# Optimization experiments

Hardware: AMD Instinct MI355X
Metric: run time of the kernel (lower is better)

The kernel has to match this reference:

```python
import jax, jax.numpy as jnp
import numpy as np

N_NODES = 100000
N_EDGES = 1600000
D_IN = 128
D_OUT = 128


def setup_inputs() -> dict:
    key = jax.random.key(0)
    k_x, k_w, k_r, k_c, k_v = jax.random.split(key, 5)
    x = jax.random.normal(k_x, (N_NODES, D_IN), dtype=jnp.float32)
    # xavier_uniform: U(-a, a), a = sqrt(6/(fan_in+fan_out))
    a = float(np.sqrt(6.0 / (D_IN + D_OUT)))
    W = jax.random.uniform(k_w, (D_IN, D_OUT), dtype=jnp.float32, minval=-a, maxval=a)
    edge_row = jax.random.randint(k_r, (N_EDGES,), 0, N_NODES, dtype=jnp.int32)
    edge_col = jax.random.randint(k_c, (N_EDGES,), 0, N_NODES, dtype=jnp.int32)
    edge_val = jax.random.uniform(k_v, (N_EDGES,), dtype=jnp.float32)
    return {"x": x, "W": W, "edge_row": edge_row, "edge_col": edge_col, "edge_val": edge_val}


def reference(x, W, edge_row, edge_col, edge_val):
    # dropout with p=0.0 is the identity (module default), so omitted.
    support = x @ W                                  # [N, D_OUT] dense GEMM
    # sparse adj @ support in COO form: out[r] += v * support[c]
    msgs = support[edge_col] * edge_val[:, None]      # [E, D_OUT] irregular gather
    out = jax.ops.segment_sum(msgs, edge_row, num_segments=x.shape[0])
    return jnp.tanh(out)
```

## Files before the change

kernel.cpp:

```cpp
#include <hip/hip_runtime.h>
#include <hip/hip_bf16.h>
#include <hip/hip_fp16.h>
#include <math.h>

#define D 128
#define BIN_SHIFT 8
#define BIN_ROWS 256
#define NB_MAX 512
#define CPAD 16
#define AW 4096

typedef _Float16 half8 __attribute__((ext_vector_type(8)));
typedef float floatx4 __attribute__((ext_vector_type(4)));
typedef float floatx2 __attribute__((ext_vector_type(2)));

__global__ void gcn_wt_kernel(const float* __restrict__ W,
                              unsigned short* __restrict__ wt,
                              int* __restrict__ cbin) {
    const int i = blockIdx.x * 256 + threadIdx.x;
    const int n = i >> 7, k = i & 127;
    wt[i] = __half_as_ushort(__float2half_rn(W[k * D + n]));
    if (blockIdx.x < 2) cbin[blockIdx.x * 256 + threadIdx.x] = 0;
}

__global__ __launch_bounds__(256) void gcn_gemm_kernel(
        const float* __restrict__ x, const unsigned short* __restrict__ wt,
        unsigned short* __restrict__ support2, int n_nodes) {
    const int wave = threadIdx.x >> 6;
    const int lane = threadIdx.x & 63;
    const int q = lane >> 4;
    const int n16 = lane & 15;
    const int row_base = blockIdx.x * 128 + wave * 32;
    if (row_base >= n_nodes) return;

    const half8* wt8 = (const half8*)wt;

    floatx4 acc[2][8];
#pragma unroll
    for (int mt = 0; mt < 2; ++mt)
#pragma unroll
        for (int nt = 0; nt < 8; ++nt) acc[mt][nt] = (floatx4){0.f, 0.f, 0.f, 0.f};

#pragma unroll
    for (int kc = 0; kc < 4; ++kc) {
        half8 b[8];
#pragma unroll
        for (int nt = 0; nt < 8; ++nt)
            b[nt] = wt8[(nt * 16 + n16) * 16 + kc * 4 + q];
#pragma unroll
        for (int mt = 0; mt < 2; ++mt) {
            const float* xp = x + (size_t)(row_base + mt * 16 + n16) * D
                                + kc * 32 + q * 8;
            const float4 f0 = *(const float4*)xp;
            const float4 f1 = *(const float4*)(xp + 4);
            half8 a;
            a[0] = (_Float16)f0.x; a[1] = (_Float16)f0.y;
            a[2] = (_Float16)f0.z; a[3] = (_Float16)f0.w;
            a[4] = (_Float16)f1.x; a[5] = (_Float16)f1.y;
            a[6] = (_Float16)f1.z; a[7] = (_Float16)f1.w;
#pragma unroll
            for (int nt = 0; nt < 8; ++nt)
                acc[mt][nt] = __builtin_amdgcn_mfma_f32_16x16x32_f16(
                    a, b[nt], acc[mt][nt], 0, 0, 0);
        }
    }

#pragma unroll
    for (int mt = 0; mt < 2; ++mt) {
        const int r0 = row_base + mt * 16 + q * 4;
#pragma unroll
        for (int nt = 0; nt < 8; ++nt) {
            const int col = nt * 16 + n16;
#pragma unroll
            for (int i = 0; i < 4; ++i)
                support2[(size_t)(r0 + i) * D + col] =
                    __half_as_ushort(__float2half_rn(acc[mt][nt][i]));
        }
    }
}

__global__ __launch_bounds__(256) void gcn_chist_kernel(
        const int* __restrict__ erow, int* __restrict__ cbin, int n_edges) {
    __shared__ int h[NB_MAX];
    const int t = threadIdx.x;
    h[t] = 0;
    h[t + 256] = 0;
    __syncthreads();
    const int stride = gridDim.x * 256 * 4;
    const int nv = n_edges & ~3;
    for (int i = (blockIdx.x * 256 + t) * 4; i + 3 < n_edges; i += stride) {
        const int4 r = *(const int4*)(erow + i);
        atomicAdd(&h[r.x >> BIN_SHIFT], 1);
        atomicAdd(&h[r.y >> BIN_SHIFT], 1);
        atomicAdd(&h[r.z >> BIN_SHIFT], 1);
        atomicAdd(&h[r.w >> BIN_SHIFT], 1);
    }
    if (blockIdx.x == 0) {
        for (int i = nv + t; i < n_edges; i += 256)
            atomicAdd(&h[erow[i] >> BIN_SHIFT], 1);
    }
    __syncthreads();
    if (h[t] > 0) atomicAdd(&cbin[t], h[t]);
    if (h[t + 256] > 0) atomicAdd(&cbin[t + 256], h[t + 256]);
}

__global__ __launch_bounds__(512) void gcn_cscan_kernel(
        const int* __restrict__ cbin, int* __restrict__ cbase,
        int* __restrict__ ccur, int* __restrict__ offsets,
        int nbins, int n_nodes, int n_edges) {
    __shared__ int sm[512];
    const int t = threadIdx.x;
    const int v = (t < nbins) ? cbin[t] : 0;
    sm[t] = v;
    __syncthreads();
    for (int off = 1; off < 512; off <<= 1) {
        int tv = (t >= off) ? sm[t - off] : 0;
        __syncthreads();
        sm[t] += tv;
        __syncthreads();
    }
    const int ex = sm[t] - v;
    if (t < nbins) { cbase[t] = ex; ccur[t * CPAD] = ex; }
    if (t == 0) { cbase[nbins] = n_edges; offsets[n_nodes] = n_edges; }
}

__global__ __launch_bounds__(512) void gcn_binA_kernel(
        const int* __restrict__ erow, const int* __restrict__ ecol,
        const float* __restrict__ eval, int* __restrict__ ccur,
        uint2* __restrict__ tmp8, int n_edges, int nbins) {
    __shared__ uint2 recs[AW];
    __shared__ int hist[NB_MAX];
    __shared__ int lstart[NB_MAX];
    __shared__ int gbase[NB_MAX];
    const int t = threadIdx.x;
    const int w0 = blockIdx.x * AW;
    const int wend = min(w0 + AW, n_edges);
    const int cnt = wend - w0;

    hist[t] = 0;
    __syncthreads();

    for (int i = w0 + t; i < wend; i += 512)
        atomicAdd(&hist[erow[i] >> BIN_SHIFT], 1);
    __syncthreads();

    {
        const int v = hist[t];
        gbase[t] = v;
        __syncthreads();
        for (int off = 1; off < 512; off <<= 1) {
            int tv = (t >= off) ? gbase[t - off] : 0;
            __syncthreads();
            gbase[t] += tv;
            __syncthreads();
        }
        lstart[t] = gbase[t] - v;
        __syncthreads();
    }

    {
        const int c = hist[t];
        int gb = 0;
        if (t < nbins && c > 0) gb = atomicAdd(&ccur[t * CPAD], c);
        __syncthreads();
        gbase[t] = gb;
        hist[t] = lstart[t];
    }
    __syncthreads();

    for (int i = w0 + t; i < wend; i += 512) {
        const int r = erow[i];
        const int c = ecol[i];
        const unsigned short vh = __half_as_ushort(__float2half_rn(eval[i]));
        const int b = r >> BIN_SHIFT;
        const int p = atomicAdd(&hist[b], 1);
        recs[p] = make_uint2(((unsigned)r << 15) | vh, (unsigned)c);
    }
    __syncthreads();

    for (int s = t; s < cnt; s += 512) {
        const uint2 rec = recs[s];
        const int b = (int)(rec.x >> 15) >> BIN_SHIFT;
        tmp8[gbase[b] + (s - lstart[b])] = rec;
    }
}

__global__ __launch_bounds__(256) void gcn_binB_kernel(
        const uint2* __restrict__ tmp8, const int* __restrict__ cbase,
        int* __restrict__ offsets,
        unsigned int* __restrict__ rec4, int n_nodes) {
    __shared__ int cnt[BIN_ROWS];
    __shared__ int sm[BIN_ROWS];
    const int bin = blockIdx.x;
    const int r0 = bin << BIN_SHIFT;
    const int t = threadIdx.x;
    cnt[t] = 0;
    __syncthreads();

    const int beg = cbase[bin];
    const int end = cbase[bin + 1];

    for (int i = beg + t; i < end; i += 256)
        atomicAdd(&cnt[(int)(tmp8[i].x >> 15) - r0], 1);
    __syncthreads();

    const int v = cnt[t];
    sm[t] = v;
    __syncthreads();
    for (int off = 1; off < 256; off <<= 1) {
        int tv = (t >= off) ? sm[t - off] : 0;
        __syncthreads();
        sm[t] += tv;
        __syncthreads();
    }
    const int mypos = beg + sm[t] - v;

    const int row = r0 + t;
    if (row < n_nodes) offsets[row] = mypos;
    __syncthreads();
    cnt[t] = mypos;
    __syncthreads();

    for (int i = beg + t; i < end; i += 256) {
        const uint2 p = tmp8[i];
        const int pos = atomicAdd(&cnt[(int)(p.x >> 15) - r0], 1);
        rec4[pos] = (p.y << 15) | (p.x & 0x7FFFu);
    }
}

__global__ __launch_bounds__(256) void gcn_gather_kernel(
        const unsigned int* __restrict__ support_u,
        const unsigned int* __restrict__ rec4,
        const int* __restrict__ offsets,
        float* __restrict__ out, int n_nodes) {
    const int node = __builtin_amdgcn_readfirstlane(
        blockIdx.x * 4 + (threadIdx.x >> 6));
    const int lane = threadIdx.x & 63;
    if (node >= n_nodes) return;

    const int beg = offsets[node];
    const int end = offsets[node + 1];

    float ax = 0.f, ay = 0.f, bx = 0.f, by = 0.f;
    int e = beg;
    for (; e + 7 < end; e += 8) {
        unsigned r[8], s[8];
#pragma unroll
        for (int j = 0; j < 8; ++j) r[j] = rec4[e + j];
#pragma unroll
        for (int j = 0; j < 8; ++j)
            s[j] = support_u[(size_t)(r[j] >> 15) * 64 + lane];
#pragma unroll
        for (int j = 0; j < 8; ++j) {
            const float v = __half2float(__ushort_as_half((unsigned short)(r[j] & 0x7FFFu)));
            const float slo = __half2float(__ushort_as_half((unsigned short)(s[j] & 0xFFFFu)));
            const float shi = __half2float(__ushort_as_half((unsigned short)(s[j] >> 16)));
            if (j & 1) { bx += v * slo; by += v * shi; }
            else       { ax += v * slo; ay += v * shi; }
        }
    }
    for (; e + 3 < end; e += 4) {
        unsigned r[4], s[4];
#pragma unroll
        for (int j = 0; j < 4; ++j) r[j] = rec4[e + j];
#pragma unroll
        for (int j = 0; j < 4; ++j)
            s[j] = support_u[(size_t)(r[j] >> 15) * 64 + lane];
#pragma unroll
        for (int j = 0; j < 4; ++j) {
            const float v = __half2float(__ushort_as_half((unsigned short)(r[j] & 0x7FFFu)));
            const float slo = __half2float(__ushort_as_half((unsigned short)(s[j] & 0xFFFFu)));
            const float shi = __half2float(__ushort_as_half((unsigned short)(s[j] >> 16)));
            if (j & 1) { bx += v * slo; by += v * shi; }
            else       { ax += v * slo; ay += v * shi; }
        }
    }
    for (; e < end; ++e) {
        const unsigned r = rec4[e];
        const unsigned s = support_u[(size_t)(r >> 15) * 64 + lane];
        const float v = __half2float(__ushort_as_half((unsigned short)(r & 0x7FFFu)));
        ax += v * __half2float(__ushort_as_half((unsigned short)(s & 0xFFFFu)));
        ay += v * __half2float(__ushort_as_half((unsigned short)(s >> 16)));
    }

    floatx2 res;
    res.x = tanhf(ax + bx);
    res.y = tanhf(ay + by);
    floatx2* out2 = (floatx2*)out;
    __builtin_nontemporal_store(res, &out2[(size_t)node * 64 + lane]);
}

extern "C" void kernel_launch(void* const* d_in, const int* in_sizes, int n_in,
                              void* d_out, int out_size, void* d_ws, size_t ws_size,
                              hipStream_t stream) {
    const float* x    = (const float*)d_in[0];
    const float* W    = (const float*)d_in[1];
    const int*   erow = (const int*)d_in[2];
    const int*   ecol = (const int*)d_in[3];
    const float* eval = (const float*)d_in[4];
    float* out = (float*)d_out;

    const int n_nodes = in_sizes[0] / D;
    const int n_edges = in_sizes[2];
    const int nbins = (n_nodes + BIN_ROWS - 1) >> BIN_SHIFT;

    unsigned short* support2 = (unsigned short*)d_ws;
    unsigned short* wt = support2 + (size_t)n_nodes * D;
    uint2* tmp8   = (uint2*)(wt + D * D);
    unsigned int* rec4 = (unsigned int*)(tmp8 + n_edges);
    int*  offsets = (int*)(rec4 + n_edges);
    int*  cbin    = offsets + n_nodes + 1;
    int*  cbase   = cbin + NB_MAX;
    int*  ccur    = cbase + NB_MAX + 1;

    gcn_wt_kernel<<<(D * D) / 256, 256, 0, stream>>>(W, wt, cbin);
    gcn_gemm_kernel<<<(n_nodes + 127) / 128, 256, 0, stream>>>(
        x, wt, support2, n_nodes);

    gcn_chist_kernel<<<320, 256, 0, stream>>>(erow, cbin, n_edges);
    gcn_cscan_kernel<<<1, 512, 0, stream>>>(cbin, cbase, ccur, offsets,
                                            nbins, n_nodes, n_edges);

    gcn_binA_kernel<<<(n_edges + AW - 1) / AW, 512, 0, stream>>>(
        erow, ecol, eval, ccur, tmp8, n_edges, nbins);
    gcn_binB_kernel<<<nbins, 256, 0, stream>>>(tmp8, cbase, offsets, rec4, n_nodes);

    gcn_gather_kernel<<<(n_nodes + 3) / 4, 256, 0, stream>>>(
        (const unsigned int*)support2, rec4, offsets, out, n_nodes);
}
```

Before: 241.3 us.

## Scatter binA records directly and gather support rows as 8-byte loads per half-wave

The binning kernel drops its shared-memory staging buffer and prefix scan. Each edge record is now written straight to its global bin slot through a shared atomic cursor, using 256 threads per block. The gather kernel splits each wave into two halves that take alternate edges, and each lane loads 8 bytes (four fp16 values) instead of 4. The two halves' partial sums are combined with a cross-half shuffle before the tanh and a 16-byte store. This aims to cut the edge-loop iterations per wave in half and to shrink binA's shared-memory footprint. The cost is less coalesced scattered global writes in binA, plus an extra shuffle and idle lanes at the store in the gather.

```diff
diff --git a/kernel.cpp b/kernel.cpp
--- a/kernel.cpp
+++ b/kernel.cpp
@@ -124,64 +124,41 @@
     if (t == 0) { cbase[nbins] = n_edges; offsets[n_nodes] = n_edges; }
 }
 
-__global__ __launch_bounds__(512) void gcn_binA_kernel(
+__global__ __launch_bounds__(256) void gcn_binA_kernel(
         const int* __restrict__ erow, const int* __restrict__ ecol,
         const float* __restrict__ eval, int* __restrict__ ccur,
         uint2* __restrict__ tmp8, int n_edges, int nbins) {
-    __shared__ uint2 recs[AW];
     __shared__ int hist[NB_MAX];
-    __shared__ int lstart[NB_MAX];
-    __shared__ int gbase[NB_MAX];
+    __shared__ int base[NB_MAX];
     const int t = threadIdx.x;
     const int w0 = blockIdx.x * AW;
     const int wend = min(w0 + AW, n_edges);
-    const int cnt = wend - w0;
 
     hist[t] = 0;
-    __syncthreads();
-
-    for (int i = w0 + t; i < wend; i += 512)
+    hist[t + 256] = 0;
+    __syncthreads();
+
+    for (int i = w0 + t; i < wend; i += 256)
         atomicAdd(&hist[erow[i] >> BIN_SHIFT], 1);
     __syncthreads();
 
-    {
-        const int v = hist[t];
-        gbase[t] = v;
-        __syncthreads();
-        for (int off = 1; off < 512; off <<= 1) {
-            int tv = (t >= off) ? gbase[t - off] : 0;
-            __syncthreads();
-            gbase[t] += tv;
-            __syncthreads();
-        }
-        lstart[t] = gbase[t] - v;
-        __syncthreads();
-    }
-
-    {
-        const int c = hist[t];
-        int gb = 0;
-        if (t < nbins && c > 0) gb = atomicAdd(&ccur[t * CPAD], c);
-        __syncthreads();
-        gbase[t] = gb;
-        hist[t] = lstart[t];
-    }
-    __syncthreads();
-
-    for (int i = w0 + t; i < wend; i += 512) {
+#pragma unroll
+    for (int s = 0; s < 2; ++s) {
+        const int b = t + s * 256;
+        const int c = hist[b];
+        base[b] = (b < nbins && c > 0) ? atomicAdd(&ccur[b * CPAD], c) : 0;
+    }
+    __syncthreads();
+    hist[t] = base[t];
+    hist[t + 256] = base[t + 256];
+    __syncthreads();
+
+    for (int i = w0 + t; i < wend; i += 256) {
         const int r = erow[i];
         const int c = ecol[i];
         const unsigned short vh = __half_as_ushort(__float2half_rn(eval[i]));
-        const int b = r >> BIN_SHIFT;
-        const int p = atomicAdd(&hist[b], 1);
-        recs[p] = make_uint2(((unsigned)r << 15) | vh, (unsigned)c);
-    }
-    __syncthreads();
-
-    for (int s = t; s < cnt; s += 512) {
-        const uint2 rec = recs[s];
-        const int b = (int)(rec.x >> 15) >> BIN_SHIFT;
-        tmp8[gbase[b] + (s - lstart[b])] = rec;
+        const int pos = atomicAdd(&hist[r >> BIN_SHIFT], 1);
+        tmp8[pos] = make_uint2(((unsigned)r << 15) | vh, (unsigned)c);
     }
 }
 
@@ -236,58 +213,70 @@
     const int node = __builtin_amdgcn_readfirstlane(
         blockIdx.x * 4 + (threadIdx.x >> 6));
     const int lane = threadIdx.x & 63;
+    const int half = lane >> 5;
+    const int l32 = lane & 31;
     if (node >= n_nodes) return;
+
+    const uint2* support8 = (const uint2*)support_u;
 
     const int beg = offsets[node];
     const int end = offsets[node + 1];
 
-    float ax = 0.f, ay = 0.f, bx = 0.f, by = 0.f;
+    float a0 = 0.f, a1 = 0.f, a2 = 0.f, a3 = 0.f;
+    float b0 = 0.f, b1 = 0.f, b2 = 0.f, b3 = 0.f;
     int e = beg;
     for (; e + 7 < end; e += 8) {
-        unsigned r[8], s[8];
-#pragma unroll
-        for (int j = 0; j < 8; ++j) r[j] = rec4[e + j];
-#pragma unroll
-        for (int j = 0; j < 8; ++j)
-            s[j] = support_u[(size_t)(r[j] >> 15) * 64 + lane];
-#pragma unroll
-        for (int j = 0; j < 8; ++j) {
-            const float v = __half2float(__ushort_as_half((unsigned short)(r[j] & 0x7FFFu)));
-            const float slo = __half2float(__ushort_as_half((unsigned short)(s[j] & 0xFFFFu)));
-            const float shi = __half2float(__ushort_as_half((unsigned short)(s[j] >> 16)));
-            if (j & 1) { bx += v * slo; by += v * shi; }
-            else       { ax += v * slo; ay += v * shi; }
-        }
-    }
-    for (; e + 3 < end; e += 4) {
-        unsigned r[4], s[4];
-#pragma unroll
-        for (int j = 0; j < 4; ++j) r[j] = rec4[e + j];
+        unsigned r[4];
+        uint2 s[4];
+#pragma unroll
+        for (int j = 0; j < 4; ++j) r[j] = rec4[e + 2 * j + half];
 #pragma unroll
         for (int j = 0; j < 4; ++j)
-            s[j] = support_u[(size_t)(r[j] >> 15) * 64 + lane];
+            s[j] = support8[(size_t)(r[j] >> 15) * 32 + l32];
 #pragma unroll
         for (int j = 0; j < 4; ++j) {
             const float v = __half2float(__ushort_as_half((unsigned short)(r[j] & 0x7FFFu)));
-            const float slo = __half2float(__ushort_as_half((unsigned short)(s[j] & 0xFFFFu)));
-            const float shi = __half2float(__ushort_as_half((unsigned short)(s[j] >> 16)));
-            if (j & 1) { bx += v * slo; by += v * shi; }
-            else       { ax += v * slo; ay += v * shi; }
+            const float c0 = __half2float(__ushort_as_half((unsigned short)(s[j].x & 0xFFFFu)));
+            const float c1 = __half2float(__ushort_as_half((unsigned short)(s[j].x >> 16)));
+            const float c2 = __half2float(__ushort_as_half((unsigned short)(s[j].y & 0xFFFFu)));
+            const float c3 = __half2float(__ushort_as_half((unsigned short)(s[j].y >> 16)));
+            if (j & 1) { b0 += v * c0; b1 += v * c1; b2 += v * c2; b3 += v * c3; }
+            else       { a0 += v * c0; a1 += v * c1; a2 += v * c2; a3 += v * c3; }
         }
     }
-    for (; e < end; ++e) {
+    for (; e + 1 < end; e += 2) {
+        const unsigned r = rec4[e + half];
+        const uint2 s = support8[(size_t)(r >> 15) * 32 + l32];
+        const float v = __half2float(__ushort_as_half((unsigned short)(r & 0x7FFFu)));
+        a0 += v * __half2float(__ushort_as_half((unsigned short)(s.x & 0xFFFFu)));
+        a1 += v * __half2float(__ushort_as_half((unsigned short)(s.x >> 16)));
+        a2 += v * __half2float(__ushort_as_half((unsigned short)(s.y & 0xFFFFu)));
+        a3 += v * __half2float(__ushort_as_half((unsigned short)(s.y >> 16)));
+    }
+    if (e < end) {
         const unsigned r = rec4[e];
-        const unsigned s = support_u[(size_t)(r >> 15) * 64 + lane];
-        const float v = __half2float(__ushort_as_half((unsigned short)(r & 0x7FFFu)));
-        ax += v * __half2float(__ushort_as_half((unsigned short)(s & 0xFFFFu)));
-        ay += v * __half2float(__ushort_as_half((unsigned short)(s >> 16)));
-    }
-
-    floatx2 res;
-    res.x = tanhf(ax + bx);
-    res.y = tanhf(ay + by);
-    floatx2* out2 = (floatx2*)out;
-    __builtin_nontemporal_store(res, &out2[(size_t)node * 64 + lane]);
+        const uint2 s = support8[(size_t)(r >> 15) * 32 + l32];
+        const float v = half ? 0.f
+            : __half2float(__ushort_as_half((unsigned short)(r & 0x7FFFu)));
+        a0 += v * __half2float(__ushort_as_half((unsigned short)(s.x & 0xFFFFu)));
+        a1 += v * __half2float(__ushort_as_half((unsigned short)(s.x >> 16)));
+        a2 += v * __half2float(__ushort_as_half((unsigned short)(s.y & 0xFFFFu)));
+        a3 += v * __half2float(__ushort_as_half((unsigned short)(s.y >> 16)));
+    }
+
+    a0 += b0; a1 += b1; a2 += b2; a3 += b3;
+    a0 += __shfl_xor(a0, 32);
+    a1 += __shfl_xor(a1, 32);
+    a2 += __shfl_xor(a2, 32);
+    a3 += __shfl_xor(a3, 32);
+
+    if (half == 0) {
+        floatx4 res;
+        res.x = tanhf(a0); res.y = tanhf(a1);
+        res.z = tanhf(a2); res.w = tanhf(a3);
+        floatx4* out4 = (floatx4*)out;
+        __builtin_nontemporal_store(res, &out4[(size_t)node * 32 + l32]);
+    }
 }
 
 extern "C" void kernel_launch(void* const* d_in, const int* in_sizes, int n_in,
@@ -321,7 +310,7 @@
     gcn_cscan_kernel<<<1, 512, 0, stream>>>(cbin, cbase, ccur, offsets,
                                             nbins, n_nodes, n_edges);
 
-    gcn_binA_kernel<<<(n_edges + AW - 1) / AW, 512, 0, stream>>>(
+    gcn_binA_kernel<<<(n_edges + AW - 1) / AW, 256, 0, stream>>>(
         erow, ecol, eval, ccur, tmp8, n_edges, nbins);
     gcn_binB_kernel<<<nbins, 256, 0, stream>>>(tmp8, cbase, offsets, rec4, n_nodes);
 
```

New measurement: 265.6 us. 1.1x slower.

## Fuse per-row sort with gather into one bin kernel using LDS records

Applied to the files above, without the earlier changes.

Halves the bin size to 128 rows (782 bins) and merges the second binning pass with the gather/tanh kernel. Each block counts and scans the rows in its bin, scatters the packed edge records into shared memory (falling back to global memory when the bin exceeds LCAP), then eight waves loop over the bin's rows doing the gather. This removes the offsets array, one kernel launch, and the global write and re-read of rec4. The cost is only 782 blocks of 512 threads for the gather phase, which may limit occupancy and latency hiding compared with the earlier one-wave-per-node launch.

```diff
diff --git a/kernel.cpp b/kernel.cpp
--- a/kernel.cpp
+++ b/kernel.cpp
@@ -4,11 +4,12 @@
 #include <math.h>
 
 #define D 128
-#define BIN_SHIFT 8
-#define BIN_ROWS 256
-#define NB_MAX 512
+#define BIN_SHIFT 7
+#define BIN_ROWS 128
+#define NB_MAX 1024
 #define CPAD 16
 #define AW 4096
+#define LCAP 2560
 
 typedef _Float16 half8 __attribute__((ext_vector_type(8)));
 typedef float floatx4 __attribute__((ext_vector_type(4)));
@@ -20,7 +21,7 @@
     const int i = blockIdx.x * 256 + threadIdx.x;
     const int n = i >> 7, k = i & 127;
     wt[i] = __half_as_ushort(__float2half_rn(W[k * D + n]));
-    if (blockIdx.x < 2) cbin[blockIdx.x * 256 + threadIdx.x] = 0;
+    if (blockIdx.x < 4) cbin[blockIdx.x * 256 + threadIdx.x] = 0;
 }
 
 __global__ __launch_bounds__(256) void gcn_gemm_kernel(
@@ -83,8 +84,8 @@
         const int* __restrict__ erow, int* __restrict__ cbin, int n_edges) {
     __shared__ int h[NB_MAX];
     const int t = threadIdx.x;
-    h[t] = 0;
-    h[t + 256] = 0;
+#pragma unroll
+    for (int s = 0; s < 4; ++s) h[t + s * 256] = 0;
     __syncthreads();
     const int stride = gridDim.x * 256 * 4;
     const int nv = n_edges & ~3;
@@ -100,20 +101,22 @@
             atomicAdd(&h[erow[i] >> BIN_SHIFT], 1);
     }
     __syncthreads();
-    if (h[t] > 0) atomicAdd(&cbin[t], h[t]);
-    if (h[t + 256] > 0) atomicAdd(&cbin[t + 256], h[t + 256]);
-}
-
-__global__ __launch_bounds__(512) void gcn_cscan_kernel(
+#pragma unroll
+    for (int s = 0; s < 4; ++s) {
+        const int b = t + s * 256;
+        if (h[b] > 0) atomicAdd(&cbin[b], h[b]);
+    }
+}
+
+__global__ __launch_bounds__(1024) void gcn_cscan_kernel(
         const int* __restrict__ cbin, int* __restrict__ cbase,
-        int* __restrict__ ccur, int* __restrict__ offsets,
-        int nbins, int n_nodes, int n_edges) {
-    __shared__ int sm[512];
+        int* __restrict__ ccur, int nbins, int n_edges) {
+    __shared__ int sm[1024];
     const int t = threadIdx.x;
     const int v = (t < nbins) ? cbin[t] : 0;
     sm[t] = v;
     __syncthreads();
-    for (int off = 1; off < 512; off <<= 1) {
+    for (int off = 1; off < 1024; off <<= 1) {
         int tv = (t >= off) ? sm[t - off] : 0;
         __syncthreads();
         sm[t] += tv;
@@ -121,7 +124,7 @@
     }
     const int ex = sm[t] - v;
     if (t < nbins) { cbase[t] = ex; ccur[t * CPAD] = ex; }
-    if (t == 0) { cbase[nbins] = n_edges; offsets[n_nodes] = n_edges; }
+    if (t == 0) cbase[nbins] = n_edges;
 }
 
 __global__ __launch_bounds__(512) void gcn_binA_kernel(
@@ -132,40 +135,46 @@
     __shared__ int hist[NB_MAX];
     __shared__ int lstart[NB_MAX];
     __shared__ int gbase[NB_MAX];
+    __shared__ int sm[512];
     const int t = threadIdx.x;
     const int w0 = blockIdx.x * AW;
     const int wend = min(w0 + AW, n_edges);
     const int cnt = wend - w0;
 
     hist[t] = 0;
+    hist[t + 512] = 0;
     __syncthreads();
 
     for (int i = w0 + t; i < wend; i += 512)
         atomicAdd(&hist[erow[i] >> BIN_SHIFT], 1);
     __syncthreads();
 
-    {
-        const int v = hist[t];
-        gbase[t] = v;
-        __syncthreads();
-        for (int off = 1; off < 512; off <<= 1) {
-            int tv = (t >= off) ? gbase[t - off] : 0;
-            __syncthreads();
-            gbase[t] += tv;
-            __syncthreads();
-        }
-        lstart[t] = gbase[t] - v;
-        __syncthreads();
-    }
-
-    {
-        const int c = hist[t];
+    const int c0 = hist[2 * t], c1 = hist[2 * t + 1];
+    const int s2 = c0 + c1;
+    sm[t] = s2;
+    __syncthreads();
+    for (int off = 1; off < 512; off <<= 1) {
+        int tv = (t >= off) ? sm[t - off] : 0;
+        __syncthreads();
+        sm[t] += tv;
+        __syncthreads();
+    }
+    const int ex = sm[t] - s2;
+    lstart[2 * t] = ex;
+    lstart[2 * t + 1] = ex + c0;
+    __syncthreads();
+
+#pragma unroll
+    for (int s = 0; s < 2; ++s) {
+        const int b = 2 * t + s;
+        const int c = hist[b];
         int gb = 0;
-        if (t < nbins && c > 0) gb = atomicAdd(&ccur[t * CPAD], c);
-        __syncthreads();
-        gbase[t] = gb;
-        hist[t] = lstart[t];
-    }
+        if (b < nbins && c > 0) gb = atomicAdd(&ccur[b * CPAD], c);
+        gbase[b] = gb;
+    }
+    __syncthreads();
+    hist[2 * t] = lstart[2 * t];
+    hist[2 * t + 1] = lstart[2 * t + 1];
     __syncthreads();
 
     for (int i = w0 + t; i < wend; i += 512) {
@@ -185,109 +194,102 @@
     }
 }
 
-__global__ __launch_bounds__(256) void gcn_binB_kernel(
+__global__ __launch_bounds__(512) void gcn_gatherB_kernel(
         const uint2* __restrict__ tmp8, const int* __restrict__ cbase,
-        int* __restrict__ offsets,
-        unsigned int* __restrict__ rec4, int n_nodes) {
-    __shared__ int cnt[BIN_ROWS];
-    __shared__ int sm[BIN_ROWS];
+        const unsigned int* __restrict__ support_u,
+        unsigned int* __restrict__ rec4,
+        float* __restrict__ out, int n_nodes) {
+    __shared__ int rcnt[BIN_ROWS];
+    __shared__ int rstart[BIN_ROWS];
+    __shared__ int ssm[BIN_ROWS];
+    __shared__ unsigned recs[LCAP];
     const int bin = blockIdx.x;
     const int r0 = bin << BIN_SHIFT;
     const int t = threadIdx.x;
-    cnt[t] = 0;
+    if (t < BIN_ROWS) rcnt[t] = 0;
     __syncthreads();
 
     const int beg = cbase[bin];
     const int end = cbase[bin + 1];
-
-    for (int i = beg + t; i < end; i += 256)
-        atomicAdd(&cnt[(int)(tmp8[i].x >> 15) - r0], 1);
-    __syncthreads();
-
-    const int v = cnt[t];
-    sm[t] = v;
-    __syncthreads();
-    for (int off = 1; off < 256; off <<= 1) {
-        int tv = (t >= off) ? sm[t - off] : 0;
-        __syncthreads();
-        sm[t] += tv;
-        __syncthreads();
-    }
-    const int mypos = beg + sm[t] - v;
-
-    const int row = r0 + t;
-    if (row < n_nodes) offsets[row] = mypos;
-    __syncthreads();
-    cnt[t] = mypos;
-    __syncthreads();
-
-    for (int i = beg + t; i < end; i += 256) {
-        const uint2 p = tmp8[i];
-        const int pos = atomicAdd(&cnt[(int)(p.x >> 15) - r0], 1);
-        rec4[pos] = (p.y << 15) | (p.x & 0x7FFFu);
-    }
-}
-
-__global__ __launch_bounds__(256) void gcn_gather_kernel(
-        const unsigned int* __restrict__ support_u,
-        const unsigned int* __restrict__ rec4,
-        const int* __restrict__ offsets,
-        float* __restrict__ out, int n_nodes) {
-    const int node = __builtin_amdgcn_readfirstlane(
-        blockIdx.x * 4 + (threadIdx.x >> 6));
-    const int lane = threadIdx.x & 63;
-    if (node >= n_nodes) return;
-
-    const int beg = offsets[node];
-    const int end = offsets[node + 1];
-
-    float ax = 0.f, ay = 0.f, bx = 0.f, by = 0.f;
-    int e = beg;
-    for (; e + 7 < end; e += 8) {
-        unsigned r[8], s[8];
-#pragma unroll
-        for (int j = 0; j < 8; ++j) r[j] = rec4[e + j];
-#pragma unroll
-        for (int j = 0; j < 8; ++j)
-            s[j] = support_u[(size_t)(r[j] >> 15) * 64 + lane];
-#pragma unroll
-        for (int j = 0; j < 8; ++j) {
-            const float v = __half2float(__ushort_as_half((unsigned short)(r[j] & 0x7FFFu)));
-            const float slo = __half2float(__ushort_as_half((unsigned short)(s[j] & 0xFFFFu)));
-            const float shi = __half2float(__ushort_as_half((unsigned short)(s[j] >> 16)));
-            if (j & 1) { bx += v * slo; by += v * shi; }
-            else       { ax += v * slo; ay += v * shi; }
-        }
-    }
-    for (; e + 3 < end; e += 4) {
-        unsigned r[4], s[4];
-#pragma unroll
-        for (int j = 0; j < 4; ++j) r[j] = rec4[e + j];
-#pragma unroll
-        for (int j = 0; j < 4; ++j)
-            s[j] = support_u[(size_t)(r[j] >> 15) * 64 + lane];
-#pragma unroll
-        for (int j = 0; j < 4; ++j) {
-            const float v = __half2float(__ushort_as_half((unsigned short)(r[j] & 0x7FFFu)));
-            const float slo = __half2float(__ushort_as_half((unsigned short)(s[j] & 0xFFFFu)));
-            const float shi = __half2float(__ushort_as_half((unsigned short)(s[j] >> 16)));
-            if (j & 1) { bx += v * slo; by += v * shi; }
-            else       { ax += v * slo; ay += v * shi; }
-        }
-    }
-    for (; e < end; ++e) {
-        const unsigned r = rec4[e];
-        const unsigned s = support_u[(size_t)(r >> 15) * 64 + lane];
-        const float v = __half2float(__ushort_as_half((unsigned short)(r & 0x7FFFu)));
-        ax += v * __half2float(__ushort_as_half((unsigned short)(s & 0xFFFFu)));
-        ay += v * __half2float(__ushort_as_half((unsigned short)(s >> 16)));
-    }
-
-    floatx2 res;
-    res.x = tanhf(ax + bx);
-    res.y = tanhf(ay + by);
-    floatx2* out2 = (floatx2*)out;
-    __builtin_nontemporal_store(res, &out2[(size_t)node * 64 + lane]);
+    const int m = end - beg;
+
+    for (int i = beg + t; i < end; i += 512)
+        atomicAdd(&rcnt[(int)(tmp8[i].x >> 15) - r0], 1);
+    __syncthreads();
+
+    if (t < BIN_ROWS) ssm[t] = rcnt[t];
+    __syncthreads();
+    for (int off = 1; off < BIN_ROWS; off <<= 1) {
+        int tv = (t >= off && t < BIN_ROWS) ? ssm[t - off] : 0;
+        __syncthreads();
+        if (t < BIN_ROWS) ssm[t] += tv;
+        __syncthreads();
+    }
+    if (t < BIN_ROWS) {
+        const int v = rcnt[t];
+        rstart[t] = ssm[t] - v;
+        rcnt[t] = ssm[t] - v;
+    }
+    __syncthreads();
+
+    const bool fast = (m <= LCAP);
+    if (fast) {
+        for (int i = beg + t; i < end; i += 512) {
+            const uint2 p = tmp8[i];
+            const int pos = atomicAdd(&rcnt[(int)(p.x >> 15) - r0], 1);
+            recs[pos] = (p.y << 15) | (p.x & 0x7FFFu);
+        }
+    } else {
+        for (int i = beg + t; i < end; i += 512) {
+            const uint2 p = tmp8[i];
+            const int pos = atomicAdd(&rcnt[(int)(p.x >> 15) - r0], 1);
+            rec4[beg + pos] = (p.y << 15) | (p.x & 0x7FFFu);
+        }
+    }
+    __syncthreads();
+
+    const unsigned* rp = fast ? (const unsigned*)recs : (rec4 + beg);
+    const int wave = t >> 6;
+    const int lane = t & 63;
+
+    for (int lr = wave; lr < BIN_ROWS; lr += 8) {
+        const int node = r0 + lr;
+        if (node >= n_nodes) break;
+        const int rs = rstart[lr];
+        const int re = rcnt[lr];
+
+        float ax = 0.f, ay = 0.f, bx = 0.f, by = 0.f;
+        int e = rs;
+        for (; e + 7 < re; e += 8) {
+            unsigned r[8], s[8];
+#pragma unroll
+            for (int j = 0; j < 8; ++j) r[j] = rp[e + j];
+#pragma unroll
+            for (int j = 0; j < 8; ++j)
+                s[j] = support_u[(size_t)(r[j] >> 15) * 64 + lane];
+#pragma unroll
+            for (int j = 0; j < 8; ++j) {
+                const float v = __half2float(__ushort_as_half((unsigned short)(r[j] & 0x7FFFu)));
+                const float slo = __half2float(__ushort_as_half((unsigned short)(s[j] & 0xFFFFu)));
+                const float shi = __half2float(__ushort_as_half((unsigned short)(s[j] >> 16)));
+                if (j & 1) { bx += v * slo; by += v * shi; }
+                else       { ax += v * slo; ay += v * shi; }
+            }
+        }
+        for (; e < re; ++e) {
+            const unsigned r = rp[e];
+            const unsigned s = support_u[(size_t)(r >> 15) * 64 + lane];
+            const float v = __half2float(__ushort_as_half((unsigned short)(r & 0x7FFFu)));
+            ax += v * __half2float(__ushort_as_half((unsigned short)(s & 0xFFFFu)));
+            ay += v * __half2float(__ushort_as_half((unsigned short)(s >> 16)));
+        }
+
+        floatx2 res;
+        res.x = tanhf(ax + bx);
+        res.y = tanhf(ay + by);
+        floatx2* out2 = (floatx2*)out;
+        __builtin_nontemporal_store(res, &out2[(size_t)node * 64 + lane]);
+    }
 }
 
 extern "C" void kernel_launch(void* const* d_in, const int* in_sizes, int n_in,
@@ -308,8 +310,7 @@
     unsigned short* wt = support2 + (size_t)n_nodes * D;
     uint2* tmp8   = (uint2*)(wt + D * D);
     unsigned int* rec4 = (unsigned int*)(tmp8 + n_edges);
-    int*  offsets = (int*)(rec4 + n_edges);
-    int*  cbin    = offsets + n_nodes + 1;
+    int*  cbin    = (int*)(rec4 + n_edges);
     int*  cbase   = cbin + NB_MAX;
     int*  ccur    = cbase + NB_MAX + 1;
 
@@ -318,13 +319,10 @@
         x, wt, support2, n_nodes);
 
     gcn_chist_kernel<<<320, 256, 0, stream>>>(erow, cbin, n_edges);
-    gcn_cscan_kernel<<<1, 512, 0, stream>>>(cbin, cbase, ccur, offsets,
-                                            nbins, n_nodes, n_edges);
+    gcn_cscan_kernel<<<1, 1024, 0, stream>>>(cbin, cbase, ccur, nbins, n_edges);
 
     gcn_binA_kernel<<<(n_edges + AW - 1) / AW, 512, 0, stream>>>(
         erow, ecol, eval, ccur, tmp8, n_edges, nbins);
-    gcn_binB_kernel<<<nbins, 256, 0, stream>>>(tmp8, cbase, offsets, rec4, n_nodes);
-
-    gcn_gather_kernel<<<(n_nodes + 3) / 4, 256, 0, stream>>>(
-        (const unsigned int*)support2, rec4, offsets, out, n_nodes);
-}
+    gcn_gatherB_kernel<<<nbins, 512, 0, stream>>>(
+        tmp8, cbase, (const unsigned int*)support2, rec4, out, n_nodes);
+}
```

After: 246.2 us. 2.0% more time.

## Fuse preprocessing and GEMM stages into one cooperative persistent kernel

Applied to the files above, without the earlier changes.

Merges the W transpose, GEMM, bin histogram, scan, and both binning passes into a single cooperative kernel separated by grid.sync, with the original separate launches kept as a fallback. The aim is to remove launch overhead and the idle tails between the six small dependent kernels, and to let the GEMM and the histogram run in the same phase. To fit 256-thread blocks, the binning window is halved and the scans now handle two bins per thread. The cost is grid-wide barriers, a grid sized by occupancy that may limit GEMM parallelism, and high shared-memory use from the 2048-entry record buffer.

```diff
diff --git a/kernel.cpp b/kernel.cpp
--- a/kernel.cpp
+++ b/kernel.cpp
@@ -1,36 +1,44 @@
 #include <hip/hip_runtime.h>
+#include <hip/hip_cooperative_groups.h>
 #include <hip/hip_bf16.h>
 #include <hip/hip_fp16.h>
 #include <math.h>
+
+namespace cg = cooperative_groups;
 
 #define D 128
 #define BIN_SHIFT 8
 #define BIN_ROWS 256
 #define NB_MAX 512
 #define CPAD 16
-#define AW 4096
+#define AW 2048
 
 typedef _Float16 half8 __attribute__((ext_vector_type(8)));
 typedef float floatx4 __attribute__((ext_vector_type(4)));
 typedef float floatx2 __attribute__((ext_vector_type(2)));
 
-__global__ void gcn_wt_kernel(const float* __restrict__ W,
-                              unsigned short* __restrict__ wt,
-                              int* __restrict__ cbin) {
-    const int i = blockIdx.x * 256 + threadIdx.x;
-    const int n = i >> 7, k = i & 127;
-    wt[i] = __half_as_ushort(__float2half_rn(W[k * D + n]));
-    if (blockIdx.x < 2) cbin[blockIdx.x * 256 + threadIdx.x] = 0;
-}
-
-__global__ __launch_bounds__(256) void gcn_gemm_kernel(
-        const float* __restrict__ x, const unsigned short* __restrict__ wt,
-        unsigned short* __restrict__ support2, int n_nodes) {
+
+__device__ __forceinline__ void wt_body(const float* __restrict__ W,
+                                        unsigned short* __restrict__ wt,
+                                        int* __restrict__ cbin,
+                                        int bid, int nblk) {
+    const int t = threadIdx.x;
+    for (int i = bid * 256 + t; i < D * D; i += nblk * 256) {
+        const int n = i >> 7, k = i & 127;
+        wt[i] = __half_as_ushort(__float2half_rn(W[k * D + n]));
+    }
+    for (int i = bid * 256 + t; i < NB_MAX; i += nblk * 256) cbin[i] = 0;
+}
+
+__device__ __forceinline__ void gemm_body(const float* __restrict__ x,
+                                          const unsigned short* __restrict__ wt,
+                                          unsigned short* __restrict__ support2,
+                                          int n_nodes, int tile) {
     const int wave = threadIdx.x >> 6;
     const int lane = threadIdx.x & 63;
     const int q = lane >> 4;
     const int n16 = lane & 15;
-    const int row_base = blockIdx.x * 128 + wave * 32;
+    const int row_base = tile * 128 + wave * 32;
     if (row_base >= n_nodes) return;
 
     const half8* wt8 = (const half8*)wt;
@@ -79,23 +87,24 @@
     }
 }
 
-__global__ __launch_bounds__(256) void gcn_chist_kernel(
-        const int* __restrict__ erow, int* __restrict__ cbin, int n_edges) {
-    __shared__ int h[NB_MAX];
+__device__ __forceinline__ void chist_body(const int* __restrict__ erow,
+                                           int* __restrict__ cbin,
+                                           int n_edges, int bid, int nblk,
+                                           int* h) {
     const int t = threadIdx.x;
     h[t] = 0;
     h[t + 256] = 0;
     __syncthreads();
-    const int stride = gridDim.x * 256 * 4;
+    const int stride = nblk * 256 * 4;
     const int nv = n_edges & ~3;
-    for (int i = (blockIdx.x * 256 + t) * 4; i + 3 < n_edges; i += stride) {
+    for (int i = (bid * 256 + t) * 4; i + 3 < n_edges; i += stride) {
         const int4 r = *(const int4*)(erow + i);
         atomicAdd(&h[r.x >> BIN_SHIFT], 1);
         atomicAdd(&h[r.y >> BIN_SHIFT], 1);
         atomicAdd(&h[r.z >> BIN_SHIFT], 1);
         atomicAdd(&h[r.w >> BIN_SHIFT], 1);
     }
-    if (blockIdx.x == 0) {
+    if (bid == 0) {
         for (int i = nv + t; i < n_edges; i += 256)
             atomicAdd(&h[erow[i] >> BIN_SHIFT], 1);
     }
@@ -104,71 +113,75 @@
     if (h[t + 256] > 0) atomicAdd(&cbin[t + 256], h[t + 256]);
 }
 
-__global__ __launch_bounds__(512) void gcn_cscan_kernel(
-        const int* __restrict__ cbin, int* __restrict__ cbase,
-        int* __restrict__ ccur, int* __restrict__ offsets,
-        int nbins, int n_nodes, int n_edges) {
-    __shared__ int sm[512];
+__device__ __forceinline__ void cscan_body(const int* __restrict__ cbin,
+                                           int* __restrict__ cbase,
+                                           int* __restrict__ ccur,
+                                           int* __restrict__ offsets,
+                                           int nbins, int n_nodes, int n_edges,
+                                           int* sm) {
     const int t = threadIdx.x;
-    const int v = (t < nbins) ? cbin[t] : 0;
-    sm[t] = v;
-    __syncthreads();
-    for (int off = 1; off < 512; off <<= 1) {
+    const int v0 = (2 * t < nbins) ? cbin[2 * t] : 0;
+    const int v1 = (2 * t + 1 < nbins) ? cbin[2 * t + 1] : 0;
+    const int s2 = v0 + v1;
+    sm[t] = s2;
+    __syncthreads();
+    for (int off = 1; off < 256; off <<= 1) {
         int tv = (t >= off) ? sm[t - off] : 0;
         __syncthreads();
         sm[t] += tv;
         __syncthreads();
     }
-    const int ex = sm[t] - v;
-    if (t < nbins) { cbase[t] = ex; ccur[t * CPAD] = ex; }
+    const int ex = sm[t] - s2;
+    if (2 * t < nbins)     { cbase[2 * t] = ex;          ccur[(2 * t) * CPAD] = ex; }
+    if (2 * t + 1 < nbins) { cbase[2 * t + 1] = ex + v0; ccur[(2 * t + 1) * CPAD] = ex + v0; }
     if (t == 0) { cbase[nbins] = n_edges; offsets[n_nodes] = n_edges; }
 }
 
-__global__ __launch_bounds__(512) void gcn_binA_kernel(
+__device__ __forceinline__ void binA_body(
         const int* __restrict__ erow, const int* __restrict__ ecol,
         const float* __restrict__ eval, int* __restrict__ ccur,
-        uint2* __restrict__ tmp8, int n_edges, int nbins) {
-    __shared__ uint2 recs[AW];
-    __shared__ int hist[NB_MAX];
-    __shared__ int lstart[NB_MAX];
-    __shared__ int gbase[NB_MAX];
+        uint2* __restrict__ tmp8, int n_edges, int nbins, int w,
+        int* hist, int* lstart, int* gbase, int* sm, uint2* recs) {
     const int t = threadIdx.x;
-    const int w0 = blockIdx.x * AW;
+    const int w0 = w * AW;
     const int wend = min(w0 + AW, n_edges);
-    const int cnt = wend - w0;
+    const int wcnt = wend - w0;
 
     hist[t] = 0;
-    __syncthreads();
-
-    for (int i = w0 + t; i < wend; i += 512)
+    hist[t + 256] = 0;
+    __syncthreads();
+
+    for (int i = w0 + t; i < wend; i += 256)
         atomicAdd(&hist[erow[i] >> BIN_SHIFT], 1);
     __syncthreads();
 
+    const int c0 = hist[2 * t], c1 = hist[2 * t + 1];
+    const int s2 = c0 + c1;
+    sm[t] = s2;
+    __syncthreads();
+    for (int off = 1; off < 256; off <<= 1) {
+        int tv = (t >= off) ? sm[t - off] : 0;
+        __syncthreads();
+        sm[t] += tv;
+        __syncthreads();
+    }
+    const int ex = sm[t] - s2;
+    lstart[2 * t] = ex;
+    lstart[2 * t + 1] = ex + c0;
+
     {
-        const int v = hist[t];
-        gbase[t] = v;
-        __syncthreads();
-        for (int off = 1; off < 512; off <<= 1) {
-            int tv = (t >= off) ? gbase[t - off] : 0;
-            __syncthreads();
-            gbase[t] += tv;
-            __syncthreads();
-        }
-        lstart[t] = gbase[t] - v;
-        __syncthreads();
-    }
-
-    {
-        const int c = hist[t];
-        int gb = 0;
-        if (t < nbins && c > 0) gb = atomicAdd(&ccur[t * CPAD], c);
-        __syncthreads();
-        gbase[t] = gb;
-        hist[t] = lstart[t];
-    }
-    __syncthreads();
-
-    for (int i = w0 + t; i < wend; i += 512) {
+        int gb0 = 0, gb1 = 0;
+        if (2 * t < nbins && c0 > 0)     gb0 = atomicAdd(&ccur[(2 * t) * CPAD], c0);
+        if (2 * t + 1 < nbins && c1 > 0) gb1 = atomicAdd(&ccur[(2 * t + 1) * CPAD], c1);
+        gbase[2 * t] = gb0;
+        gbase[2 * t + 1] = gb1;
+    }
+    __syncthreads();
+    hist[2 * t] = lstart[2 * t];
+    hist[2 * t + 1] = lstart[2 * t + 1];
+    __syncthreads();
+
+    for (int i = w0 + t; i < wend; i += 256) {
         const int r = erow[i];
         const int c = ecol[i];
         const unsigned short vh = __half_as_ushort(__float2half_rn(eval[i]));
@@ -178,20 +191,18 @@
     }
     __syncthreads();
 
-    for (int s = t; s < cnt; s += 512) {
+    for (int s = t; s < wcnt; s += 256) {
         const uint2 rec = recs[s];
         const int b = (int)(rec.x >> 15) >> BIN_SHIFT;
         tmp8[gbase[b] + (s - lstart[b])] = rec;
     }
-}
-
-__global__ __launch_bounds__(256) void gcn_binB_kernel(
+    __syncthreads();
+}
+
+__device__ __forceinline__ void binB_body(
         const uint2* __restrict__ tmp8, const int* __restrict__ cbase,
-        int* __restrict__ offsets,
-        unsigned int* __restrict__ rec4, int n_nodes) {
-    __shared__ int cnt[BIN_ROWS];
-    __shared__ int sm[BIN_ROWS];
-    const int bin = blockIdx.x;
+        int* __restrict__ offsets, unsigned int* __restrict__ rec4,
+        int n_nodes, int bin, int* cnt, int* sm) {
     const int r0 = bin << BIN_SHIFT;
     const int t = threadIdx.x;
     cnt[t] = 0;
@@ -226,6 +237,92 @@
         const int pos = atomicAdd(&cnt[(int)(p.x >> 15) - r0], 1);
         rec4[pos] = (p.y << 15) | (p.x & 0x7FFFu);
     }
+    __syncthreads();
+}
+
+__global__ __launch_bounds__(256) void gcn_mega_kernel(
+        const float* __restrict__ x, const float* __restrict__ W,
+        unsigned short* __restrict__ wt, unsigned short* __restrict__ support2,
+        const int* __restrict__ erow, const int* __restrict__ ecol,
+        const float* __restrict__ eval,
+        int* __restrict__ cbin, int* __restrict__ cbase, int* __restrict__ ccur,
+        int* __restrict__ offsets, uint2* __restrict__ tmp8,
+        unsigned int* __restrict__ rec4,
+        int n_nodes, int n_edges, int nbins) {
+    __shared__ uint2 recs[AW];
+    __shared__ int smA[NB_MAX];
+    __shared__ int smB[NB_MAX];
+    __shared__ int smC[NB_MAX];
+    __shared__ int smD[256];
+    cg::grid_group grid = cg::this_grid();
+    const int bid = blockIdx.x, nblk = gridDim.x;
+
+    wt_body(W, wt, cbin, bid, nblk);
+    grid.sync();
+
+    for (int tile = bid; tile * 128 < n_nodes; tile += nblk)
+        gemm_body(x, wt, support2, n_nodes, tile);
+    chist_body(erow, cbin, n_edges, bid, nblk, smA);
+    grid.sync();
+
+    if (bid == 0)
+        cscan_body(cbin, cbase, ccur, offsets, nbins, n_nodes, n_edges, smD);
+    grid.sync();
+
+    for (int w = bid; w * AW < n_edges; w += nblk)
+        binA_body(erow, ecol, eval, ccur, tmp8, n_edges, nbins, w,
+                  smA, smB, smC, smD, recs);
+    grid.sync();
+
+    for (int b = bid; b < nbins; b += nblk)
+        binB_body(tmp8, cbase, offsets, rec4, n_nodes, b, smA, smB);
+}
+
+__global__ __launch_bounds__(256) void gcn_wt_kernel(
+        const float* __restrict__ W, unsigned short* __restrict__ wt,
+        int* __restrict__ cbin) {
+    wt_body(W, wt, cbin, blockIdx.x, gridDim.x);
+}
+__global__ __launch_bounds__(256) void gcn_gemm_kernel(
+        const float* __restrict__ x, const unsigned short* __restrict__ wt,
+        unsigned short* __restrict__ support2, int n_nodes) {
+    for (int tile = blockIdx.x; tile * 128 < n_nodes; tile += gridDim.x)
+        gemm_body(x, wt, support2, n_nodes, tile);
+}
+__global__ __launch_bounds__(256) void gcn_chist_kernel(
+        const int* __restrict__ erow, int* __restrict__ cbin, int n_edges) {
+    __shared__ int smA[NB_MAX];
+    chist_body(erow, cbin, n_edges, blockIdx.x, gridDim.x, smA);
+}
+__global__ __launch_bounds__(256) void gcn_cscan_kernel(
+        const int* __restrict__ cbin, int* __restrict__ cbase,
+        int* __restrict__ ccur, int* __restrict__ offsets,
+        int nbins, int n_nodes, int n_edges) {
+    __shared__ int smD[256];
+    if (blockIdx.x == 0)
+        cscan_body(cbin, cbase, ccur, offsets, nbins, n_nodes, n_edges, smD);
+}
+__global__ __launch_bounds__(256) void gcn_binA_kernel(
+        const int* __restrict__ erow, const int* __restrict__ ecol,
+        const float* __restrict__ eval, int* __restrict__ ccur,
+        uint2* __restrict__ tmp8, int n_edges, int nbins) {
+    __shared__ uint2 recs[AW];
+    __shared__ int smA[NB_MAX];
+    __shared__ int smB[NB_MAX];
+    __shared__ int smC[NB_MAX];
+    __shared__ int smD[256];
+    for (int w = blockIdx.x; w * AW < n_edges; w += gridDim.x)
+        binA_body(erow, ecol, eval, ccur, tmp8, n_edges, nbins, w,
+                  smA, smB, smC, smD, recs);
+}
+__global__ __launch_bounds__(256) void gcn_binB_kernel(
+        const uint2* __restrict__ tmp8, const int* __restrict__ cbase,
+        int* __restrict__ offsets, unsigned int* __restrict__ rec4,
+        int n_nodes, int nbins) {
+    __shared__ int smA[NB_MAX];
+    __shared__ int smB[NB_MAX];
+    for (int b = blockIdx.x; b < nbins; b += gridDim.x)
+        binB_body(tmp8, cbase, offsets, rec4, n_nodes, b, smA, smB);
 }
 
 __global__ __launch_bounds__(256) void gcn_gather_kernel(
@@ -313,17 +410,42 @@
     int*  cbase   = cbin + NB_MAX;
     int*  ccur    = cbase + NB_MAX + 1;
 
-    gcn_wt_kernel<<<(D * D) / 256, 256, 0, stream>>>(W, wt, cbin);
-    gcn_gemm_kernel<<<(n_nodes + 127) / 128, 256, 0, stream>>>(
-        x, wt, support2, n_nodes);
-
-    gcn_chist_kernel<<<320, 256, 0, stream>>>(erow, cbin, n_edges);
-    gcn_cscan_kernel<<<1, 512, 0, stream>>>(cbin, cbase, ccur, offsets,
-                                            nbins, n_nodes, n_edges);
-
-    gcn_binA_kernel<<<(n_edges + AW - 1) / AW, 512, 0, stream>>>(
-        erow, ecol, eval, ccur, tmp8, n_edges, nbins);
-    gcn_binB_kernel<<<nbins, 256, 0, stream>>>(tmp8, cbase, offsets, rec4, n_nodes);
+    static int coopGrid = -1;
+    if (coopGrid < 0) {
+        int dev = 0;
+        hipGetDevice(&dev);
+        int numCU = 0, coop = 0, maxB = 0;
+        hipDeviceGetAttribute(&numCU, hipDeviceAttributeMultiprocessorCount, dev);
+        hipDeviceGetAttribute(&coop, hipDeviceAttributeCooperativeLaunch, dev);
+        hipOccupancyMaxActiveBlocksPerMultiprocessor(&maxB, gcn_mega_kernel, 256, 0);
+        coopGrid = (coop && numCU > 0 && maxB > 0) ? numCU * maxB : 0;
+    }
+
+    bool mega_ok = false;
+    if (coopGrid > 0) {
+        void* kargs[] = {
+            (void*)&x, (void*)&W, (void*)&wt, (void*)&support2,
+            (void*)&erow, (void*)&ecol, (void*)&eval,
+            (void*)&cbin, (void*)&cbase, (void*)&ccur, (void*)&offsets,
+            (void*)&tmp8, (void*)&rec4,
+            (void*)&n_nodes, (void*)&n_edges, (void*)&nbins };
+        mega_ok = (hipLaunchCooperativeKernel(
+                       reinterpret_cast<void*>(gcn_mega_kernel),
+                       dim3(coopGrid), dim3(256), kargs, 0, stream) == hipSuccess);
+    }
+
+    if (!mega_ok) {
+        gcn_wt_kernel<<<64, 256, 0, stream>>>(W, wt, cbin);
+        gcn_gemm_kernel<<<(n_nodes + 127) / 128, 256, 0, stream>>>(
+            x, wt, support2, n_nodes);
+        gcn_chist_kernel<<<320, 256, 0, stream>>>(erow, cbin, n_edges);
+        gcn_cscan_kernel<<<1, 256, 0, stream>>>(cbin, cbase, ccur, offsets,
+                                                nbins, n_nodes, n_edges);
+        gcn_binA_kernel<<<(n_edges + AW - 1) / AW, 256, 0, stream>>>(
+            erow, ecol, eval, ccur, tmp8, n_edges, nbins);
+        gcn_binB_kernel<<<nbins, 256, 0, stream>>>(tmp8, cbase, offsets, rec4,
+                                                   n_nodes, nbins);
+    }
 
     gcn_gather_kernel<<<(n_nodes + 3) / 4, 256, 0, stream>>>(
         (const unsigned int*)support2, rec4, offsets, out, n_nodes);
```

Measured after the change: 376.4 us. 56.0% more time.
